# Performance work log

Measured on AMD Instinct MI355X. Metric: run time of the kernel, lower is better.

Reference implementation:

```python
import jax, jax.numpy as jnp
import numpy as np

B, Q, T, D, FD, H, N, FF = 64, 64, 448, 512, 1024, 8, 2, 2048
S = Q + T
DH = D // H
EPS = 1e-12


def _ln(x, g, b):
    m = jnp.mean(x, -1, keepdims=True)
    v = jnp.mean((x - m) ** 2, -1, keepdims=True)
    return (x - m) / jnp.sqrt(v + EPS) * g + b


def _sinusoidal(n_pos, dim):
    j = np.arange(dim)
    pos = np.arange(n_pos)[:, None]
    angle = pos / np.power(10000.0, 2 * (j // 2) / dim)
    pe = np.zeros((n_pos, dim), dtype=np.float32)
    pe[:, 0::2] = np.sin(angle[:, 0::2])
    pe[:, 1::2] = np.cos(angle[:, 1::2])
    return jnp.asarray(pe)


def setup_inputs() -> dict:
    key = jax.random.key(0)
    ks = iter(jax.random.split(key, 40))
    s = 0.02
    rn = lambda *shape: jax.random.normal(next(ks), shape, jnp.float32) * s
    inp = {
        'video': jax.random.normal(next(ks), (B, T, FD), jnp.float32),
        'question': jax.random.normal(next(ks), (B, Q, D), jnp.float32),
        'mask': jnp.ones((B, S), jnp.int32),
        'pos_emb': _sinusoidal(S, D),
        'mod_emb': rn(2, D),
        'Wv': rn(FD, D), 'bv': jnp.zeros((D,), jnp.float32),
        'nv_g': jnp.ones((D,), jnp.float32), 'nv_b': jnp.zeros((D,), jnp.float32),
        'emb_g': jnp.ones((D,), jnp.float32), 'emb_b': jnp.zeros((D,), jnp.float32),
        'Wq': rn(N, D, D), 'bq': jnp.zeros((N, D), jnp.float32),
        'Wk': rn(N, D, D), 'bk': jnp.zeros((N, D), jnp.float32),
        'Wva': rn(N, D, D), 'bva': jnp.zeros((N, D), jnp.float32),
        'Wo': rn(N, D, D), 'bo': jnp.zeros((N, D), jnp.float32),
        'ln1_g': jnp.ones((N, D), jnp.float32), 'ln1_b': jnp.zeros((N, D), jnp.float32),
        'W1': rn(N, D, FF), 'b1': jnp.zeros((N, FF), jnp.float32),
        'W2': rn(N, FF, D), 'b2': jnp.zeros((N, D), jnp.float32),
        'ln2_g': jnp.ones((N, D), jnp.float32), 'ln2_b': jnp.zeros((N, D), jnp.float32),
    }
    return inp


def reference(video, question, mask, pos_emb, mod_emb, Wv, bv, nv_g, nv_b,
              emb_g, emb_b, Wq, bq, Wk, bk, Wva, bva, Wo, bo,
              ln1_g, ln1_b, W1, b1, W2, b2, ln2_g, ln2_b):
    # project + norm video features
    v = _ln(video @ Wv + bv, nv_g, nv_b)                      # [B,T,D]
    x = jnp.concatenate([question, v], axis=1)                # [B,S,D]
    mod_ids = jnp.concatenate([jnp.zeros(Q, jnp.int32), jnp.ones(T, jnp.int32)])
    x = x + pos_emb[None] + mod_emb[mod_ids][None]
    x = _ln(x, emb_g, emb_b)

    pad = (mask == 0)[:, None, None, :]                       # [B,1,1,S]
    scale = 1.0 / jnp.sqrt(jnp.asarray(DH, x.dtype))
    split = lambda t: t.reshape(B, S, H, DH).transpose(0, 2, 1, 3)  # [B,H,S,DH]

    for i in range(N):
        q = split(x @ Wq[i] + bq[i]) * scale
        k = split(x @ Wk[i] + bk[i])
        vv = split(x @ Wva[i] + bva[i])
        scores = jnp.einsum('bhqd,bhkd->bhqk', q, k)          # [B,H,S,S]
        scores = jnp.where(pad, -jnp.inf, scores)
        w = jax.nn.softmax(scores, axis=-1)
        ctx = jnp.einsum('bhqk,bhkd->bhqd', w, vv)
        ctx = ctx.transpose(0, 2, 1, 3).reshape(B, S, D)
        x = _ln(ctx @ Wo[i] + bo[i] + x, ln1_g[i], ln1_b[i])
        h = jax.nn.gelu(x @ W1[i] + b1[i], approximate=False)
        x = _ln(h @ W2[i] + b2[i] + x, ln2_g[i], ln2_b[i])
    return x
```

## Files before the change

kernel.cpp:

```cpp
#include <hip/hip_runtime.h>
#include <hip/hip_bf16.h>
#include <stdint.h>

#define Bb 64
#define Qq 64
#define Tt 448
#define Dd 512
#define FDd 1024
#define Hh 8
#define NL 2
#define FFf 2048
#define Ss 512
#define DHh 64

typedef unsigned short u16;
typedef __bf16 bf16x8 __attribute__((ext_vector_type(8)));
typedef float f32x4 __attribute__((ext_vector_type(4)));
typedef u16 u16x4 __attribute__((ext_vector_type(4)));

__device__ __forceinline__ float bf2f(u16 u) { return __uint_as_float(((uint32_t)u) << 16); }
__device__ __forceinline__ u16 f2bfu(float f) {
    __bf16 h = (__bf16)f;
    return __builtin_bit_cast(unsigned short, h);
}
__device__ __forceinline__ float ldx(const void* p, long i, int isbf) {
    return isbf ? bf2f(((const u16*)p)[i]) : ((const float*)p)[i];
}
__device__ __forceinline__ float geluf(float v) {
    float u = v * (1.0f + 0.044715f * v * v) * -1.5957691216057308f;
    return v / (1.0f + __expf(u));
}
__device__ __forceinline__ void gload16(const void* g, void* l) {
    __builtin_amdgcn_global_load_lds((const __attribute__((address_space(1))) void*)g,
                                     (__attribute__((address_space(3))) void*)l, 16, 0, 0);
}
#define MFMA16(a, b, c) __builtin_amdgcn_mfma_f32_16x16x32_bf16(a, b, c, 0, 0, 0)

__global__ void probe_kernel(const void* pos_emb, int* flag) {
    if (threadIdx.x == 0) {
        uint32_t w = *(const uint32_t*)pos_emb;
        *flag = (w == 0x3F800000u) ? 1 : 0;
    }
}

__global__ void convert_kernel(const void* __restrict__ src, u16* __restrict__ dst, long n,
                               const int* __restrict__ flag) {
    const int isbf = *flag;
    if (isbf) return;
    long i = (long)blockIdx.x * blockDim.x + threadIdx.x;
    long stride = (long)gridDim.x * blockDim.x;
    for (; i < n; i += stride) {
        dst[i] = f2bfu(((const float*)src)[i]);
    }
}

__global__ void transpose_kernel(const void* __restrict__ src, u16* __restrict__ dst,
                                 int R, int C, long elem_off, const int* __restrict__ flag) {
    __shared__ u16 tile[32][33];
    const int isbf = *flag;
    const int c0 = blockIdx.x * 32, r0 = blockIdx.y * 32;
    const int tx = threadIdx.x, ty = threadIdx.y;
#pragma unroll
    for (int i = 0; i < 32; i += 8) {
        long idx = elem_off + (long)(r0 + ty + i) * C + (c0 + tx);
        tile[ty + i][tx] = isbf ? ((const u16*)src)[idx] : f2bfu(((const float*)src)[idx]);
    }
    __syncthreads();
#pragma unroll
    for (int i = 0; i < 32; i += 8) {
        dst[(long)(c0 + ty + i) * R + (r0 + tx)] = tile[tx][ty + i];
    }
}

__global__ void transpose4_kernel(const void* __restrict__ s0, const void* __restrict__ s1,
                                  const void* __restrict__ s2, const void* __restrict__ s3,
                                  u16* __restrict__ d0p, u16* __restrict__ d1p,
                                  u16* __restrict__ d2p, u16* __restrict__ d3p, long elem_off,
                                  const int* __restrict__ flag) {
    __shared__ u16 tile[32][33];
    const int isbf = *flag;
    const int z = blockIdx.z;
    const void* src = (z == 0) ? s0 : (z == 1) ? s1 : (z == 2) ? s2 : s3;
    u16* dst = (z == 0) ? d0p : (z == 1) ? d1p : (z == 2) ? d2p : d3p;
    const int c0 = blockIdx.x * 32, r0 = blockIdx.y * 32;
    const int tx = threadIdx.x, ty = threadIdx.y;
#pragma unroll
    for (int i = 0; i < 32; i += 8) {
        long idx = elem_off + (long)(r0 + ty + i) * Dd + (c0 + tx);
        tile[ty + i][tx] = isbf ? ((const u16*)src)[idx] : f2bfu(((const float*)src)[idx]);
    }
    __syncthreads();
#pragma unroll
    for (int i = 0; i < 32; i += 8) {
        dst[(long)(c0 + ty + i) * Dd + (r0 + tx)] = tile[tx][ty + i];
    }
}

template <int MH>
__device__ __forceinline__ void ld_a(bf16x8 (&af)[4][2], const u16* sa, int wm, int col16,
                                     int cp0, int cp1) {
#pragma unroll
    for (int mi = 0; mi < 4; mi++) {
        int rr = wm * 128 + MH * 64 + mi * 16 + col16;
        af[mi][0] = *(const bf16x8*)&sa[rr * 64 + cp0 * 8];
        af[mi][1] = *(const bf16x8*)&sa[rr * 64 + cp1 * 8];
    }
}
template <int NH>
__device__ __forceinline__ void ld_b(bf16x8 (&bfr)[2][2][2], const u16* sb, int wn, int col16,
                                     int cp0, int cp1) {
#pragma unroll
    for (int ni = 0; ni < 2; ni++) {
        int rr = wn * 64 + NH * 32 + ni * 16 + col16;
        bfr[NH][ni][0] = *(const bf16x8*)&sb[rr * 64 + cp0 * 8];
        bfr[NH][ni][1] = *(const bf16x8*)&sb[rr * 64 + cp1 * 8];
    }
}
template <int MH, int NH>
__device__ __forceinline__ void mma4(f32x4 (&acc)[8][4], const bf16x8 (&af)[4][2],
                                     const bf16x8 (&bfr)[2][2][2]) {
#pragma unroll
    for (int mi = 0; mi < 4; mi++)
#pragma unroll
        for (int ni = 0; ni < 2; ni++)
#pragma unroll
            for (int ks = 0; ks < 2; ks++)
                acc[MH * 4 + mi][NH * 2 + ni] =
                    MFMA16(af[mi][ks], bfr[NH][ni][ks], acc[MH * 4 + mi][NH * 2 + ni]);
}

#define PH_TAIL(MH, NH)                                       \
    __builtin_amdgcn_sched_barrier(0);                        \
    __builtin_amdgcn_s_barrier();                             \
    asm volatile("s_waitcnt lgkmcnt(0)" ::: "memory");        \
    __builtin_amdgcn_sched_barrier(0);                        \
    __builtin_amdgcn_s_setprio(1);                            \
    mma4<MH, NH>(acc, af, bfr);                               \
    __builtin_amdgcn_s_setprio(0);                            \
    __builtin_amdgcn_sched_barrier(0);

template <int MODE, int KK>
__global__ __launch_bounds__(512) void gemm256(const u16* __restrict__ A,
                                               const void* __restrict__ Araw,
                                               const u16* __restrict__ Bt,
                                               const void* __restrict__ bias, long bias_off,
                                               void* __restrict__ out, int M, int N,
                                               const int* __restrict__ flag) {
    constexpr int NT = KK / 64;
    __shared__ __align__(16) u16 sA2[2][16384];
    __shared__ __align__(16) u16 sB2[2][16384];
    const int tid = threadIdx.x;
    const int lane = tid & 63, wave = tid >> 6;
    const int wm = wave >> 2, wn = wave & 3;
    const int col16 = lane & 15, quad = lane >> 4;
    const int cp0 = quad ^ (col16 & 7);
    const int cp1 = cp0 ^ 4;
    const long m0 = (long)blockIdx.y * 256;
    const long n0 = (long)blockIdx.x * 256;
    const int isbf = *flag;
    const u16* Ap = (Araw && isbf) ? (const u16*)Araw : A;

    const int g = (tid & 7) ^ ((tid >> 3) & 7);
    const u16* agbase = Ap + (m0 + (tid >> 3)) * KK + g * 8;
    const u16* bgbase = Bt + (n0 + (tid >> 3)) * KK + g * 8;

    auto stA = [&](int kt2, int q) {
        if (kt2 < NT)
            gload16(agbase + (long)q * (64LL * KK) + (long)kt2 * 64,
                    &sA2[kt2 & 1][q * 4096 + wave * 512]);
    };
    auto stB = [&](int kt2, int q) {
        if (kt2 < NT)
            gload16(bgbase + (long)q * (64LL * KK) + (long)kt2 * 64,
                    &sB2[kt2 & 1][q * 4096 + wave * 512]);
    };

    f32x4 acc[8][4];
#pragma unroll
    for (int i = 0; i < 8; i++)
#pragma unroll
        for (int j = 0; j < 4; j++) acc[i][j] = (f32x4){0.f, 0.f, 0.f, 0.f};

    stA(0, 0); stA(0, 1); stA(0, 2); stA(0, 3);
    stB(0, 0); stB(0, 1); stB(0, 2); stB(0, 3);
    stB(1, 0); stB(1, 1); stB(1, 2); stB(1, 3);
    asm volatile("s_waitcnt vmcnt(4)" ::: "memory");
    __builtin_amdgcn_s_barrier();

    bf16x8 af[4][2];
    bf16x8 bfr[2][2][2];

#pragma unroll 2
    for (int kt = 0; kt < NT; ++kt) {
        const u16* sa = &sA2[kt & 1][0];
        const u16* sb = &sB2[kt & 1][0];
        ld_a<0>(af, sa, wm, col16, cp0, cp1);
        ld_b<0>(bfr, sb, wn, col16, cp0, cp1);
        stA(kt + 1, 0);
        stA(kt + 1, 1);
        PH_TAIL(0, 0)
        __builtin_amdgcn_s_barrier();
        ld_b<1>(bfr, sb, wn, col16, cp0, cp1);
        stA(kt + 1, 2);
        stA(kt + 1, 3);
        PH_TAIL(0, 1)
        __builtin_amdgcn_s_barrier();
        ld_a<1>(af, sa, wm, col16, cp0, cp1);
        stB(kt + 2, 0);
        stB(kt + 2, 1);
        PH_TAIL(1, 0)
        __builtin_amdgcn_s_barrier();
        stB(kt + 2, 2);
        stB(kt + 2, 3);
        PH_TAIL(1, 1)
        if (kt + 2 < NT)
            asm volatile("s_waitcnt vmcnt(4)" ::: "memory");
        else if (kt + 1 < NT)
            asm volatile("s_waitcnt vmcnt(0)" ::: "memory");
        __builtin_amdgcn_s_barrier();
    }

    float bb[4];
#pragma unroll
    for (int ni = 0; ni < 4; ni++)
        bb[ni] = ldx(bias, bias_off + n0 + wn * 64 + ni * 16 + col16, isbf);
#pragma unroll
    for (int mi = 0; mi < 8; mi++) {
#pragma unroll
        for (int ni = 0; ni < 4; ni++) {
            long col = n0 + wn * 64 + ni * 16 + col16;
#pragma unroll
            for (int r = 0; r < 4; r++) {
                long row = m0 + wm * 128 + mi * 16 + quad * 4 + r;
                float v = acc[mi][ni][r] + bb[ni];
                if (MODE == 0) {
                    ((u16*)out)[row * N + col] = f2bfu(v);
                } else {
                    ((u16*)out)[row * N + col] = f2bfu(geluf(v));
                }
            }
        }
    }
}

__global__ __launch_bounds__(256) void qkv_kernel(const u16* __restrict__ A,
                                                  const u16* __restrict__ Bt,
                                                  const void* __restrict__ bq,
                                                  const void* __restrict__ bk,
                                                  const void* __restrict__ bva, long boff,
                                                  u16* __restrict__ qb, u16* __restrict__ kb,
                                                  u16* __restrict__ vtb,
                                                  const int* __restrict__ flag) {
    __shared__ __align__(16) u16 sA[128 * 32];
    __shared__ __align__(16) u16 sB[128 * 32];
    const int tid = threadIdx.x;
    const int lane = tid & 63, wave = tid >> 6;
    const int wm = wave >> 1, wn = wave & 1;
    const int col16 = lane & 15, quad = lane >> 4;
    const long m0 = (long)blockIdx.y * 128;
    const long n0 = (long)blockIdx.x * 128;
    const int KK = Dd;

    f32x4 acc[4][4];
#pragma unroll
    for (int i = 0; i < 4; i++)
#pragma unroll
        for (int j = 0; j < 4; j++) acc[i][j] = (f32x4){0.f, 0.f, 0.f, 0.f};

    const int sr = tid >> 2, skq = tid & 3;
    const int ssg = skq ^ ((sr >> 1) & 3);
    const int sr2 = (tid + 256) >> 2;
    const int ssg2 = skq ^ ((sr2 >> 1) & 3);

#pragma unroll
    for (int k0 = 0; k0 < KK; k0 += 32) {
        __syncthreads();
        {
            int lbase = (wave * 64) * 8;
            gload16(&A[(m0 + sr) * KK + k0 + ssg * 8], &sA[lbase]);
            gload16(&Bt[(n0 + sr) * KK + k0 + ssg * 8], &sB[lbase]);
            int lbase2 = (256 + wave * 64) * 8;
            gload16(&A[(m0 + sr2) * KK + k0 + ssg2 * 8], &sA[lbase2]);
            gload16(&Bt[(n0 + sr2) * KK + k0 + ssg2 * 8], &sB[lbase2]);
        }
        __syncthreads();
        bf16x8 af[4], bfv[4];
#pragma unroll
        for (int mi = 0; mi < 4; mi++) {
            int rr = wm * 64 + mi * 16 + col16;
            af[mi] = *(const bf16x8*)&sA[(rr * 4 + (quad ^ ((rr >> 1) & 3))) * 8];
        }
#pragma unroll
        for (int ni = 0; ni < 4; ni++) {
            int rr = wn * 64 + ni * 16 + col16;
            bfv[ni] = *(const bf16x8*)&sB[(rr * 4 + (quad ^ ((rr >> 1) & 3))) * 8];
        }
#pragma unroll
        for (int mi = 0; mi < 4; mi++)
#pragma unroll
            for (int ni = 0; ni < 4; ni++)
                acc[mi][ni] = MFMA16(af[mi], bfv[ni], acc[mi][ni]);
    }

    const int isbf = *flag;
    const int region = (int)(n0 >> 9);
    const void* bias = (region == 0) ? bq : (region == 1) ? bk : bva;
    float bb[4];
#pragma unroll
    for (int ni = 0; ni < 4; ni++) {
        long col = n0 + wn * 64 + ni * 16 + col16;
        bb[ni] = ldx(bias, boff + (col & 511), isbf);
    }

#pragma unroll
    for (int mi = 0; mi < 4; mi++) {
#pragma unroll
        for (int ni = 0; ni < 4; ni++) {
            long col = n0 + wn * 64 + ni * 16 + col16;
            long cc = col & 511;
            long h = cc >> 6, dh = cc & 63;
            long row0 = m0 + wm * 64 + mi * 16 + quad * 4;
            long b = row0 >> 9, s0 = row0 & 511;
            if (region == 0) {
#pragma unroll
                for (int r = 0; r < 4; r++)
                    qb[(((b * 8 + h) * 512) + s0 + r) * 64 + dh] =
                        f2bfu((acc[mi][ni][r] + bb[ni]) * 0.125f);
            } else if (region == 1) {
#pragma unroll
                for (int r = 0; r < 4; r++)
                    kb[(((b * 8 + h) * 512) + s0 + r) * 64 + dh] = f2bfu(acc[mi][ni][r] + bb[ni]);
            } else {
                u16x4 pk;
#pragma unroll
                for (int r = 0; r < 4; r++) pk[r] = f2bfu(acc[mi][ni][r] + bb[ni]);
                *(u16x4*)&vtb[(((b * 8 + h) * 64) + dh) * 512 + s0] = pk;
            }
        }
    }
}

__device__ __forceinline__ float wredsum(float v) {
#pragma unroll
    for (int off = 1; off < 64; off <<= 1) v += __shfl_xor(v, off);
    return v;
}
__device__ __forceinline__ void ln8(float v[8]) {
    float s = 0.f;
#pragma unroll
    for (int j = 0; j < 8; j++) s += v[j];
    s = wredsum(s);
    float m = s * (1.0f / 512.0f);
    float q = 0.f;
#pragma unroll
    for (int j = 0; j < 8; j++) {
        v[j] -= m;
        q += v[j] * v[j];
    }
    q = wredsum(q);
    float inv = rsqrtf(q * (1.0f / 512.0f) + 1e-12f);
#pragma unroll
    for (int j = 0; j < 8; j++) v[j] *= inv;
}

__global__ __launch_bounds__(256) void embed_kernel(
    const void* __restrict__ question, const void* __restrict__ pos, const void* __restrict__ mod,
    const u16* __restrict__ tmp, const void* __restrict__ nvg, const void* __restrict__ nvb,
    const void* __restrict__ eg, const void* __restrict__ eb, u16* __restrict__ x,
    const int* __restrict__ flag) {
    const int isbf = *flag;
    const int wave = threadIdx.x >> 6, lane = threadIdx.x & 63;
    const long row = (long)blockIdx.x * 4 + wave;
    const int b = (int)(row >> 9), s = (int)(row & 511);
    const int d0 = lane * 4, d1 = 256 + lane * 4;
    float v[8];
    if (s < Qq) {
        long base = ((long)b * Qq + s) * Dd;
#pragma unroll
        for (int j = 0; j < 4; j++) {
            v[j] = ldx(question, base + d0 + j, isbf);
            v[4 + j] = ldx(question, base + d1 + j, isbf);
        }
    } else {
        const u16* tr = tmp + ((long)b * Tt + (s - Qq)) * Dd;
        u16x4 f0 = *(const u16x4*)(tr + d0);
        u16x4 f1 = *(const u16x4*)(tr + d1);
#pragma unroll
        for (int j = 0; j < 4; j++) {
            v[j] = bf2f(f0[j]);
            v[4 + j] = bf2f(f1[j]);
        }
        ln8(v);
#pragma unroll
        for (int j = 0; j < 4; j++) {
            v[j] = v[j] * ldx(nvg, d0 + j, isbf) + ldx(nvb, d0 + j, isbf);
            v[4 + j] = v[4 + j] * ldx(nvg, d1 + j, isbf) + ldx(nvb, d1 + j, isbf);
        }
    }
    const int mid = (s < Qq) ? 0 : 1;
#pragma unroll
    for (int j = 0; j < 4; j++) {
        v[j] += ldx(pos, (long)s * Dd + d0 + j, isbf) + ldx(mod, (long)mid * Dd + d0 + j, isbf);
        v[4 + j] += ldx(pos, (long)s * Dd + d1 + j, isbf) + ldx(mod, (long)mid * Dd + d1 + j, isbf);
    }
    ln8(v);
#pragma unroll
    for (int j = 0; j < 4; j++) {
        x[row * Dd + d0 + j] = f2bfu(v[j] * ldx(eg, d0 + j, isbf) + ldx(eb, d0 + j, isbf));
        x[row * Dd + d1 + j] = f2bfu(v[4 + j] * ldx(eg, d1 + j, isbf) + ldx(eb, d1 + j, isbf));
    }
}

__global__ __launch_bounds__(256) void add_ln_kernel(const u16* __restrict__ tmp,
                                                     const u16* __restrict__ xin,
                                                     const void* __restrict__ g,
                                                     const void* __restrict__ bta, long goff,
                                                     void* __restrict__ dst, int dst_is_final,
                                                     const int* __restrict__ flag) {
    const int isbf = *flag;
    const int wave = threadIdx.x >> 6, lane = threadIdx.x & 63;
    const long row = (long)blockIdx.x * 4 + wave;
// ... 151 lines not shown
        for (int dt = 0; dt < 4; dt++) {
#pragma unroll
            for (int r = 0; r < 4; r++) {
                float v = acc[t][dt][r] / accl[t][r];
                int sq = qbase + t * 16 + quad * 4 + r;
                int d = h * 64 + dt * 16 + col16;
                ctx[((long)b * Ss + sq) * Dd + d] = f2bfu(v);
            }
        }
}

extern "C" void kernel_launch(void* const* d_in, const int* in_sizes, int n_in, void* d_out,
                              int out_size, void* d_ws, size_t ws_size, hipStream_t stream) {
    const void* video = d_in[0];
    const void* question = d_in[1];
    const int* mask = (const int*)d_in[2];
    const void* pos_emb = d_in[3];
    const void* mod_emb = d_in[4];
    const void* Wv = d_in[5];
    const void* bv = d_in[6];
    const void* nv_g = d_in[7];
    const void* nv_b = d_in[8];
    const void* emb_g = d_in[9];
    const void* emb_b = d_in[10];
    const void* Wq = d_in[11];
    const void* bq = d_in[12];
    const void* Wk = d_in[13];
    const void* bk = d_in[14];
    const void* Wva = d_in[15];
    const void* bva = d_in[16];
    const void* Wo = d_in[17];
    const void* bo = d_in[18];
    const void* ln1_g = d_in[19];
    const void* ln1_b = d_in[20];
    const void* W1 = d_in[21];
    const void* b1 = d_in[22];
    const void* W2 = d_in[23];
    const void* b2 = d_in[24];
    const void* ln2_g = d_in[25];
    const void* ln2_b = d_in[26];

    char* wsb = (char*)d_ws;
    size_t off = 0;
    auto alloc = [&](size_t bytes) -> void* {
        void* p = (void*)(wsb + off);
        off += (bytes + 4095) & ~((size_t)4095);
        return p;
    };
    int* flag = (int*)alloc(16);
    u16* WvT = (u16*)alloc((size_t)Dd * FDd * 2);
    u16 *WqkvT[NL], *WoT[NL], *W1T[NL], *W2T[NL];
    for (int i = 0; i < NL; i++) {
        WqkvT[i] = (u16*)alloc((size_t)3 * Dd * Dd * 2);
        WoT[i] = (u16*)alloc((size_t)Dd * Dd * 2);
        W1T[i] = (u16*)alloc((size_t)FFf * Dd * 2);
        W2T[i] = (u16*)alloc((size_t)Dd * FFf * 2);
    }
    u16* x = (u16*)alloc((size_t)Bb * Ss * Dd * 2);
    u16* tmp = (u16*)alloc((size_t)Bb * Ss * Dd * 2);
    char* uni = (char*)alloc((size_t)134217728);
    u16* videob = (u16*)uni;
    u16* qb = (u16*)uni;
    u16* kb = (u16*)(uni + 33554432);
    u16* vtb = (u16*)(uni + 67108864);
    u16* ctxb = (u16*)(uni + 100663296);
    u16* hb = (u16*)uni;

    dim3 tb(32, 8);

    probe_kernel<<<dim3(1), dim3(64), 0, stream>>>(pos_emb, flag);
    convert_kernel<<<dim3(8192), dim3(256), 0, stream>>>(video, videob, (long)Bb * Tt * FDd, flag);

    transpose_kernel<<<dim3(Dd / 32, FDd / 32), tb, 0, stream>>>(Wv, WvT, FDd, Dd, 0L, flag);
    for (int i = 0; i < NL; i++) {
        transpose4_kernel<<<dim3(Dd / 32, Dd / 32, 4), tb, 0, stream>>>(
            Wq, Wk, Wva, Wo, WqkvT[i], WqkvT[i] + (size_t)Dd * Dd,
            WqkvT[i] + (size_t)2 * Dd * Dd, WoT[i], (long)i * Dd * Dd, flag);
        transpose_kernel<<<dim3(FFf / 32, Dd / 32), tb, 0, stream>>>(W1, W1T[i], Dd, FFf,
                                                                     (long)i * Dd * FFf, flag);
        transpose_kernel<<<dim3(Dd / 32, FFf / 32), tb, 0, stream>>>(W2, W2T[i], FFf, Dd,
                                                                     (long)i * FFf * Dd, flag);
    }

    gemm256<0, FDd><<<dim3(2, 112), dim3(512), 0, stream>>>(videob, video, WvT, bv, 0L, tmp,
                                                            Bb * Tt, Dd, flag);
    embed_kernel<<<dim3((Bb * Ss) / 4), dim3(256), 0, stream>>>(question, pos_emb, mod_emb, tmp,
                                                                nv_g, nv_b, emb_g, emb_b, x, flag);

    for (int i = 0; i < NL; i++) {
        qkv_kernel<<<dim3(12, 256), dim3(256), 0, stream>>>(x, WqkvT[i], bq, bk, bva,
                                                            (long)i * Dd, qb, kb, vtb, flag);
        flash_kernel<<<dim3(2048), dim3(256), 0, stream>>>(qb, kb, vtb, mask, ctxb);
        gemm256<0, Dd><<<dim3(2, 128), dim3(512), 0, stream>>>(ctxb, nullptr, WoT[i], bo,
                                                               (long)i * Dd, tmp, Bb * Ss, Dd,
                                                               flag);
        add_ln_kernel<<<dim3((Bb * Ss) / 4), dim3(256), 0, stream>>>(tmp, x, ln1_g, ln1_b,
                                                                     (long)i * Dd, x, 0, flag);
        gemm256<1, Dd><<<dim3(8, 128), dim3(512), 0, stream>>>(x, nullptr, W1T[i], b1,
                                                               (long)i * FFf, hb, Bb * Ss, FFf,
                                                               flag);
        gemm256<0, FFf><<<dim3(2, 128), dim3(512), 0, stream>>>(hb, nullptr, W2T[i], b2,
                                                                (long)i * Dd, tmp, Bb * Ss, Dd,
                                                                flag);
        void* dst = (i == NL - 1) ? d_out : (void*)x;
        add_ln_kernel<<<dim3((Bb * Ss) / 4), dim3(256), 0, stream>>>(
            tmp, x, ln2_g, ln2_b, (long)i * Dd, dst, (i == NL - 1) ? 1 : 0, flag);
    }
    (void)in_sizes; (void)n_in; (void)out_size; (void)ws_size;
}
```

Before: 1.339 ms.

## Use 256x256 pipelined GEMM for QKV and add XCD-aware block swizzle

Replaces the simple 128x128 single-buffered QKV GEMM with the same double-buffered 256x256 pipelined core used by the other GEMMs, shared through a macro. All GEMMs now launch a 1D grid and remap block IDs so that consecutive M tiles land on the same XCD, aiming to improve L2 reuse of A rows and weight tiles. The output width becomes a template parameter. Risks include fewer blocks for QKV (768 vs 3072) reducing occupancy, and the remap assumes M/256 is divisible by 8.

```diff
diff --git a/kernel.cpp b/kernel.cpp
--- a/kernel.cpp
+++ b/kernel.cpp
@@ -129,96 +129,100 @@
                     MFMA16(af[mi][ks], bfr[NH][ni][ks], acc[MH * 4 + mi][NH * 2 + ni]);
 }
 
-#define PH_TAIL(MH, NH)                                       \
-    __builtin_amdgcn_sched_barrier(0);                        \
-    __builtin_amdgcn_s_barrier();                             \
-    asm volatile("s_waitcnt lgkmcnt(0)" ::: "memory");        \
-    __builtin_amdgcn_sched_barrier(0);                        \
-    __builtin_amdgcn_s_setprio(1);                            \
-    mma4<MH, NH>(acc, af, bfr);                               \
-    __builtin_amdgcn_s_setprio(0);                            \
+#define PH_TAIL(MH, NH)                                \
+    __builtin_amdgcn_sched_barrier(0);                 \
+    __builtin_amdgcn_s_barrier();                      \
+    asm volatile("s_waitcnt lgkmcnt(0)" ::: "memory"); \
+    __builtin_amdgcn_sched_barrier(0);                 \
+    __builtin_amdgcn_s_setprio(1);                     \
+    mma4<MH, NH>(acc, af, bfr);                        \
+    __builtin_amdgcn_s_setprio(0);                     \
     __builtin_amdgcn_sched_barrier(0);
 
-template <int MODE, int KK>
+#define GEMM256_CORE(APTR, BPTR, KK_, NT_)                                                    \
+    const int tid = threadIdx.x;                                                              \
+    const int lane = tid & 63, wave = tid >> 6;                                               \
+    const int wm = wave >> 2, wn = wave & 3;                                                  \
+    const int col16 = lane & 15, quad = lane >> 4;                                            \
+    const int cp0 = quad ^ (col16 & 7);                                                       \
+    const int cp1 = cp0 ^ 4;                                                                  \
+    const int g = (tid & 7) ^ ((tid >> 3) & 7);                                               \
+    const u16* agbase = (APTR) + (m0 + (tid >> 3)) * (KK_) + g * 8;                           \
+    const u16* bgbase = (BPTR) + (n0 + (tid >> 3)) * (KK_) + g * 8;                           \
+    auto stA = [&](int kt2, int q) {                                                          \
+        if (kt2 < (NT_))                                                                      \
+            gload16(agbase + (long)q * (64LL * (KK_)) + (long)kt2 * 64,                       \
+                    &sA2[kt2 & 1][q * 4096 + wave * 512]);                                    \
+    };                                                                                        \
+    auto stB = [&](int kt2, int q) {                                                          \
+        if (kt2 < (NT_))                                                                      \
+            gload16(bgbase + (long)q * (64LL * (KK_)) + (long)kt2 * 64,                       \
+                    &sB2[kt2 & 1][q * 4096 + wave * 512]);                                    \
+    };                                                                                        \
+    f32x4 acc[8][4];                                                                          \
+    _Pragma("unroll") for (int i = 0; i < 8; i++) _Pragma("unroll") for (int j = 0; j < 4;    \
+                                                                         j++) acc[i][j] =    \
+        (f32x4){0.f, 0.f, 0.f, 0.f};                                                          \
+    stA(0, 0); stA(0, 1); stA(0, 2); stA(0, 3);                                               \
+    stB(0, 0); stB(0, 1); stB(0, 2); stB(0, 3);                                               \
+    stB(1, 0); stB(1, 1); stB(1, 2); stB(1, 3);                                               \
+    asm volatile("s_waitcnt vmcnt(4)" ::: "memory");                                          \
+    __builtin_amdgcn_s_barrier();                                                             \
+    bf16x8 af[4][2];                                                                          \
+    bf16x8 bfr[2][2][2];                                                                      \
+    _Pragma("unroll 2") for (int kt = 0; kt < (NT_); ++kt) {                                  \
+        const u16* sa = &sA2[kt & 1][0];                                                      \
+        const u16* sb = &sB2[kt & 1][0];                                                      \
+        ld_a<0>(af, sa, wm, col16, cp0, cp1);                                                 \
+        ld_b<0>(bfr, sb, wn, col16, cp0, cp1);                                                \
+        stA(kt + 1, 0);                                                                       \
+        stA(kt + 1, 1);                                                                       \
+        PH_TAIL(0, 0)                                                                         \
+        __builtin_amdgcn_s_barrier();                                                         \
+        ld_b<1>(bfr, sb, wn, col16, cp0, cp1);                                                \
+        stA(kt + 1, 2);                                                                       \
+        stA(kt + 1, 3);                                                                       \
+        PH_TAIL(0, 1)                                                                         \
+        __builtin_amdgcn_s_barrier();                                                         \
+        ld_a<1>(af, sa, wm, col16, cp0, cp1);                                                 \
+        stB(kt + 2, 0);                                                                       \
+        stB(kt + 2, 1);                                                                       \
+        PH_TAIL(1, 0)                                                                         \
+        __builtin_amdgcn_s_barrier();                                                         \
+        stB(kt + 2, 2);                                                                       \
+        stB(kt + 2, 3);                                                                       \
+        PH_TAIL(1, 1)                                                                         \
+        if (kt + 2 < (NT_))                                                                   \
+            asm volatile("s_waitcnt vmcnt(4)" ::: "memory");                                  \
+        else if (kt + 1 < (NT_))                                                              \
+            asm volatile("s_waitcnt vmcnt(0)" ::: "memory");                                  \
+        __builtin_amdgcn_s_barrier();                                                         \
+    }
+
+template <int MODE, int KK, int NN>
 __global__ __launch_bounds__(512) void gemm256(const u16* __restrict__ A,
                                                const void* __restrict__ Araw,
                                                const u16* __restrict__ Bt,
                                                const void* __restrict__ bias, long bias_off,
-                                               void* __restrict__ out, int M, int N,
+                                               void* __restrict__ out, int M,
                                                const int* __restrict__ flag) {
     constexpr int NT = KK / 64;
+    constexpr int nbn = NN >> 8;
     __shared__ __align__(16) u16 sA2[2][16384];
     __shared__ __align__(16) u16 sB2[2][16384];
-    const int tid = threadIdx.x;
-    const int lane = tid & 63, wave = tid >> 6;
-    const int wm = wave >> 2, wn = wave & 3;
-    const int col16 = lane & 15, quad = lane >> 4;
-    const int cp0 = quad ^ (col16 & 7);
-    const int cp1 = cp0 ^ 4;
-    const long m0 = (long)blockIdx.y * 256;
-    const long n0 = (long)blockIdx.x * 256;
     const int isbf = *flag;
     const u16* Ap = (Araw && isbf) ? (const u16*)Araw : A;
 
-    const int g = (tid & 7) ^ ((tid >> 3) & 7);
-    const u16* agbase = Ap + (m0 + (tid >> 3)) * KK + g * 8;
-    const u16* bgbase = Bt + (n0 + (tid >> 3)) * KK + g * 8;
-
-    auto stA = [&](int kt2, int q) {
-        if (kt2 < NT)
-            gload16(agbase + (long)q * (64LL * KK) + (long)kt2 * 64,
-                    &sA2[kt2 & 1][q * 4096 + wave * 512]);
-    };
-    auto stB = [&](int kt2, int q) {
-        if (kt2 < NT)
-            gload16(bgbase + (long)q * (64LL * KK) + (long)kt2 * 64,
-                    &sB2[kt2 & 1][q * 4096 + wave * 512]);
-    };
-
-    f32x4 acc[8][4];
-#pragma unroll
-    for (int i = 0; i < 8; i++)
-#pragma unroll
-        for (int j = 0; j < 4; j++) acc[i][j] = (f32x4){0.f, 0.f, 0.f, 0.f};
-
-    stA(0, 0); stA(0, 1); stA(0, 2); stA(0, 3);
-    stB(0, 0); stB(0, 1); stB(0, 2); stB(0, 3);
-    stB(1, 0); stB(1, 1); stB(1, 2); stB(1, 3);
-    asm volatile("s_waitcnt vmcnt(4)" ::: "memory");
-    __builtin_amdgcn_s_barrier();
-
-    bf16x8 af[4][2];
-    bf16x8 bfr[2][2][2];
-
-#pragma unroll 2
-    for (int kt = 0; kt < NT; ++kt) {
-        const u16* sa = &sA2[kt & 1][0];
-        const u16* sb = &sB2[kt & 1][0];
-        ld_a<0>(af, sa, wm, col16, cp0, cp1);
-        ld_b<0>(bfr, sb, wn, col16, cp0, cp1);
-        stA(kt + 1, 0);
-        stA(kt + 1, 1);
-        PH_TAIL(0, 0)
-        __builtin_amdgcn_s_barrier();
-        ld_b<1>(bfr, sb, wn, col16, cp0, cp1);
-        stA(kt + 1, 2);
-        stA(kt + 1, 3);
-        PH_TAIL(0, 1)
-        __builtin_amdgcn_s_barrier();
-        ld_a<1>(af, sa, wm, col16, cp0, cp1);
-        stB(kt + 2, 0);
-        stB(kt + 2, 1);
-        PH_TAIL(1, 0)
-        __builtin_amdgcn_s_barrier();
-        stB(kt + 2, 2);
-        stB(kt + 2, 3);
-        PH_TAIL(1, 1)
-        if (kt + 2 < NT)
-            asm volatile("s_waitcnt vmcnt(4)" ::: "memory");
-        else if (kt + 1 < NT)
-            asm volatile("s_waitcnt vmcnt(0)" ::: "memory");
-        __builtin_amdgcn_s_barrier();
-    }
+    const int bid = blockIdx.x;
+    const int xcd = bid & 7;
+    const int loc = bid >> 3;
+    const int chunk = (M >> 8) >> 3;
+    const int mloc = loc / nbn;
+    const int nloc = loc - mloc * nbn;
+    const long m0 = (long)(xcd * chunk + mloc) << 8;
+    const long n0 = (long)nloc << 8;
+
+    GEMM256_CORE(Ap, Bt, KK, NT)
 
     float bb[4];
 #pragma unroll
@@ -234,75 +238,41 @@
                 long row = m0 + wm * 128 + mi * 16 + quad * 4 + r;
                 float v = acc[mi][ni][r] + bb[ni];
                 if (MODE == 0) {
-                    ((u16*)out)[row * N + col] = f2bfu(v);
+                    ((u16*)out)[row * NN + col] = f2bfu(v);
                 } else {
-                    ((u16*)out)[row * N + col] = f2bfu(geluf(v));
+                    ((u16*)out)[row * NN + col] = f2bfu(geluf(v));
                 }
             }
         }
     }
 }
 
-__global__ __launch_bounds__(256) void qkv_kernel(const u16* __restrict__ A,
-                                                  const u16* __restrict__ Bt,
-                                                  const void* __restrict__ bq,
-                                                  const void* __restrict__ bk,
-                                                  const void* __restrict__ bva, long boff,
-                                                  u16* __restrict__ qb, u16* __restrict__ kb,
-                                                  u16* __restrict__ vtb,
-                                                  const int* __restrict__ flag) {
-    __shared__ __align__(16) u16 sA[128 * 32];
-    __shared__ __align__(16) u16 sB[128 * 32];
-    const int tid = threadIdx.x;
-    const int lane = tid & 63, wave = tid >> 6;
-    const int wm = wave >> 1, wn = wave & 1;
-    const int col16 = lane & 15, quad = lane >> 4;
-    const long m0 = (long)blockIdx.y * 128;
-    const long n0 = (long)blockIdx.x * 128;
-    const int KK = Dd;
-
-    f32x4 acc[4][4];
-#pragma unroll
-    for (int i = 0; i < 4; i++)
-#pragma unroll
-        for (int j = 0; j < 4; j++) acc[i][j] = (f32x4){0.f, 0.f, 0.f, 0.f};
-
-    const int sr = tid >> 2, skq = tid & 3;
-    const int ssg = skq ^ ((sr >> 1) & 3);
-    const int sr2 = (tid + 256) >> 2;
-    const int ssg2 = skq ^ ((sr2 >> 1) & 3);
-
-#pragma unroll
-    for (int k0 = 0; k0 < KK; k0 += 32) {
-        __syncthreads();
-        {
-            int lbase = (wave * 64) * 8;
-            gload16(&A[(m0 + sr) * KK + k0 + ssg * 8], &sA[lbase]);
-            gload16(&Bt[(n0 + sr) * KK + k0 + ssg * 8], &sB[lbase]);
-            int lbase2 = (256 + wave * 64) * 8;
-            gload16(&A[(m0 + sr2) * KK + k0 + ssg2 * 8], &sA[lbase2]);
-            gload16(&Bt[(n0 + sr2) * KK + k0 + ssg2 * 8], &sB[lbase2]);
-        }
-        __syncthreads();
-        bf16x8 af[4], bfv[4];
-#pragma unroll
-        for (int mi = 0; mi < 4; mi++) {
-            int rr = wm * 64 + mi * 16 + col16;
-            af[mi] = *(const bf16x8*)&sA[(rr * 4 + (quad ^ ((rr >> 1) & 3))) * 8];
-        }
-#pragma unroll
-        for (int ni = 0; ni < 4; ni++) {
-            int rr = wn * 64 + ni * 16 + col16;
-            bfv[ni] = *(const bf16x8*)&sB[(rr * 4 + (quad ^ ((rr >> 1) & 3))) * 8];
-        }
-#pragma unroll
-        for (int mi = 0; mi < 4; mi++)
-#pragma unroll
-            for (int ni = 0; ni < 4; ni++)
-                acc[mi][ni] = MFMA16(af[mi], bfv[ni], acc[mi][ni]);
-    }
-
+__global__ __launch_bounds__(512) void qkv256(const u16* __restrict__ A,
+                                              const u16* __restrict__ Bt,
+                                              const void* __restrict__ bq,
+                                              const void* __restrict__ bk,
+                                              const void* __restrict__ bva, long boff,
+                                              u16* __restrict__ qb, u16* __restrict__ kb,
+                                              u16* __restrict__ vtb,
+                                              const int* __restrict__ flag) {
+    constexpr int KK = Dd;
+    constexpr int NT = KK / 64;
+    constexpr int nbn = 6;
+    __shared__ __align__(16) u16 sA2[2][16384];
+    __shared__ __align__(16) u16 sB2[2][16384];
     const int isbf = *flag;
+
+    const int bid = blockIdx.x;
+    const int xcd = bid & 7;
+    const int loc = bid >> 3;
+    const int chunk = 16;
+    const int mloc = loc / nbn;
+    const int nloc = loc - mloc * nbn;
+    const long m0 = (long)(xcd * chunk + mloc) << 8;
+    const long n0 = (long)nloc << 8;
+
+    GEMM256_CORE(A, Bt, KK, NT)
+
     const int region = (int)(n0 >> 9);
     const void* bias = (region == 0) ? bq : (region == 1) ? bk : bva;
     float bb[4];
@@ -313,13 +283,13 @@
     }
 
 #pragma unroll
-    for (int mi = 0; mi < 4; mi++) {
+    for (int mi = 0; mi < 8; mi++) {
 #pragma unroll
         for (int ni = 0; ni < 4; ni++) {
             long col = n0 + wn * 64 + ni * 16 + col16;
             long cc = col & 511;
             long h = cc >> 6, dh = cc & 63;
-            long row0 = m0 + wm * 64 + mi * 16 + quad * 4;
+            long row0 = m0 + wm * 128 + mi * 16 + quad * 4;
             long b = row0 >> 9, s0 = row0 & 511;
             if (region == 0) {
 #pragma unroll
@@ -654,26 +624,26 @@
                                                                      (long)i * FFf * Dd, flag);
     }
 
-    gemm256<0, FDd><<<dim3(2, 112), dim3(512), 0, stream>>>(videob, video, WvT, bv, 0L, tmp,
-                                                            Bb * Tt, Dd, flag);
+    gemm256<0, FDd, Dd><<<dim3(112 * 2), dim3(512), 0, stream>>>(videob, video, WvT, bv, 0L, tmp,
+                                                                 Bb * Tt, flag);
     embed_kernel<<<dim3((Bb * Ss) / 4), dim3(256), 0, stream>>>(question, pos_emb, mod_emb, tmp,
                                                                 nv_g, nv_b, emb_g, emb_b, x, flag);
 
     for (int i = 0; i < NL; i++) {
-        qkv_kernel<<<dim3(12, 256), dim3(256), 0, stream>>>(x, WqkvT[i], bq, bk, bva,
-                                                            (long)i * Dd, qb, kb, vtb, flag);
+        qkv256<<<dim3(128 * 6), dim3(512), 0, stream>>>(x, WqkvT[i], bq, bk, bva, (long)i * Dd,
+                                                        qb, kb, vtb, flag);
         flash_kernel<<<dim3(2048), dim3(256), 0, stream>>>(qb, kb, vtb, mask, ctxb);
-        gemm256<0, Dd><<<dim3(2, 128), dim3(512), 0, stream>>>(ctxb, nullptr, WoT[i], bo,
-                                                               (long)i * Dd, tmp, Bb * Ss, Dd,
-                                                               flag);
+        gemm256<0, Dd, Dd><<<dim3(128 * 2), dim3(512), 0, stream>>>(ctxb, nullptr, WoT[i], bo,
+                                                                    (long)i * Dd, tmp, Bb * Ss,
+                                                                    flag);
         add_ln_kernel<<<dim3((Bb * Ss) / 4), dim3(256), 0, stream>>>(tmp, x, ln1_g, ln1_b,
                                                                      (long)i * Dd, x, 0, flag);
-        gemm256<1, Dd><<<dim3(8, 128), dim3(512), 0, stream>>>(x, nullptr, W1T[i], b1,
-                                                               (long)i * FFf, hb, Bb * Ss, FFf,
-                                                               flag);
-        gemm256<0, FFf><<<dim3(2, 128), dim3(512), 0, stream>>>(hb, nullptr, W2T[i], b2,
-                                                                (long)i * Dd, tmp, Bb * Ss, Dd,
-                                                                flag);
+        gemm256<1, Dd, FFf><<<dim3(128 * 8), dim3(512), 0, stream>>>(x, nullptr, W1T[i], b1,
+                                                                     (long)i * FFf, hb, Bb * Ss,
+                                                                     flag);
+        gemm256<0, FFf, Dd><<<dim3(128 * 2), dim3(512), 0, stream>>>(hb, nullptr, W2T[i], b2,
+                                                                     (long)i * Dd, tmp, Bb * Ss,
+                                                                     flag);
         void* dst = (i == NL - 1) ? d_out : (void*)x;
         add_ln_kernel<<<dim3((Bb * Ss) / 4), dim3(256), 0, stream>>>(
             tmp, x, ln2_g, ln2_b, (long)i * Dd, dst, (i == NL - 1) ? 1 : 0, flag);
```

Result: faster. 1.281 ms (-4.3%).

## Unify GEMMs into persistent XCD-aware 256x256 kernel with QKV epilogue and prefetch

Applied to the files above, without the earlier changes.

Replaces the separate 128x128 QKV kernel with the 256x256 pipelined GEMM, using a new epilogue mode that scatters Q (pre-scaled), K and transposed V. Block indices are remapped so each XCD works on a contiguous band of M. The W1 GEMM makes each block loop over four M tiles, reusing the pipeline and emitting an epilogue per tile. LDS fragment reads are issued earlier, with partial lgkmcnt waits and a second A-fragment buffer, to overlap them with MFMA. The aims are better L2 locality, higher MFMA efficiency for QKV and less LDS latency exposure, at the cost of more registers and fewer blocks for W1.

```diff
diff --git a/kernel.cpp b/kernel.cpp
--- a/kernel.cpp
+++ b/kernel.cpp
@@ -97,13 +97,13 @@
 }
 
 template <int MH>
-__device__ __forceinline__ void ld_a(bf16x8 (&af)[4][2], const u16* sa, int wm, int col16,
+__device__ __forceinline__ void ld_a(bf16x8 (&dst)[4][2], const u16* sa, int wm, int col16,
                                      int cp0, int cp1) {
 #pragma unroll
     for (int mi = 0; mi < 4; mi++) {
         int rr = wm * 128 + MH * 64 + mi * 16 + col16;
-        af[mi][0] = *(const bf16x8*)&sa[rr * 64 + cp0 * 8];
-        af[mi][1] = *(const bf16x8*)&sa[rr * 64 + cp1 * 8];
+        dst[mi][0] = *(const bf16x8*)&sa[rr * 64 + cp0 * 8];
+        dst[mi][1] = *(const bf16x8*)&sa[rr * 64 + cp1 * 8];
     }
 }
 template <int NH>
@@ -117,7 +117,7 @@
     }
 }
 template <int MH, int NH>
-__device__ __forceinline__ void mma4(f32x4 (&acc)[8][4], const bf16x8 (&af)[4][2],
+__device__ __forceinline__ void mma4(f32x4 (&acc)[8][4], const bf16x8 (&a)[4][2],
                                      const bf16x8 (&bfr)[2][2][2]) {
 #pragma unroll
     for (int mi = 0; mi < 4; mi++)
@@ -126,27 +126,28 @@
 #pragma unroll
             for (int ks = 0; ks < 2; ks++)
                 acc[MH * 4 + mi][NH * 2 + ni] =
-                    MFMA16(af[mi][ks], bfr[NH][ni][ks], acc[MH * 4 + mi][NH * 2 + ni]);
-}
-
-#define PH_TAIL(MH, NH)                                       \
+                    MFMA16(a[mi][ks], bfr[NH][ni][ks], acc[MH * 4 + mi][NH * 2 + ni]);
+}
+
+#define PH_CNT(MH, NH, AARR, CNT)                             \
     __builtin_amdgcn_sched_barrier(0);                        \
     __builtin_amdgcn_s_barrier();                             \
-    asm volatile("s_waitcnt lgkmcnt(0)" ::: "memory");        \
+    asm volatile("s_waitcnt lgkmcnt(" #CNT ")" ::: "memory"); \
     __builtin_amdgcn_sched_barrier(0);                        \
     __builtin_amdgcn_s_setprio(1);                            \
-    mma4<MH, NH>(acc, af, bfr);                               \
+    mma4<MH, NH>(acc, AARR, bfr);                             \
     __builtin_amdgcn_s_setprio(0);                            \
     __builtin_amdgcn_sched_barrier(0);
 
-template <int MODE, int KK>
-__global__ __launch_bounds__(512) void gemm256(const u16* __restrict__ A,
-                                               const void* __restrict__ Araw,
-                                               const u16* __restrict__ Bt,
-                                               const void* __restrict__ bias, long bias_off,
-                                               void* __restrict__ out, int M, int N,
-                                               const int* __restrict__ flag) {
+template <int MODE, int KK, int NN, int MSUB>
+__global__ __launch_bounds__(512) void gemm256(
+    const u16* __restrict__ A, const void* __restrict__ Araw, const u16* __restrict__ Bt,
+    const void* __restrict__ b0, const void* __restrict__ b1, const void* __restrict__ b2,
+    long boff, void* __restrict__ o0, void* __restrict__ o1, void* __restrict__ o2, int M,
+    const int* __restrict__ flag) {
     constexpr int NT = KK / 64;
+    constexpr int TOT = NT * MSUB;
+    constexpr int nbn = NN >> 8;
     __shared__ __align__(16) u16 sA2[2][16384];
     __shared__ __align__(16) u16 sB2[2][16384];
     const int tid = threadIdx.x;
@@ -155,24 +156,36 @@
     const int col16 = lane & 15, quad = lane >> 4;
     const int cp0 = quad ^ (col16 & 7);
     const int cp1 = cp0 ^ 4;
-    const long m0 = (long)blockIdx.y * 256;
-    const long n0 = (long)blockIdx.x * 256;
     const int isbf = *flag;
     const u16* Ap = (Araw && isbf) ? (const u16*)Araw : A;
+
+    const int bid = blockIdx.x;
+    const int xcd = bid & 7;
+    const int loc = bid >> 3;
+    const int nbm = M / (256 * MSUB);
+    const int chunk = nbm >> 3;
+    const int mloc = loc / nbn;
+    const int nloc = loc - mloc * nbn;
+    const long m0 = (long)(xcd * chunk + mloc) * (256L * MSUB);
+    const long n0 = (long)nloc << 8;
 
     const int g = (tid & 7) ^ ((tid >> 3) & 7);
     const u16* agbase = Ap + (m0 + (tid >> 3)) * KK + g * 8;
     const u16* bgbase = Bt + (n0 + (tid >> 3)) * KK + g * 8;
 
-    auto stA = [&](int kt2, int q) {
-        if (kt2 < NT)
-            gload16(agbase + (long)q * (64LL * KK) + (long)kt2 * 64,
-                    &sA2[kt2 & 1][q * 4096 + wave * 512]);
+    auto stA = [&](int s2, int q) {
+        if (s2 < TOT) {
+            const long mt = s2 / NT;
+            const long k0 = (long)(s2 & (NT - 1)) * 64;
+            gload16(agbase + mt * (256LL * KK) + (long)q * (64LL * KK) + k0,
+                    &sA2[s2 & 1][q * 4096 + wave * 512]);
+        }
     };
-    auto stB = [&](int kt2, int q) {
-        if (kt2 < NT)
-            gload16(bgbase + (long)q * (64LL * KK) + (long)kt2 * 64,
-                    &sB2[kt2 & 1][q * 4096 + wave * 512]);
+    auto stB = [&](int s2, int q) {
+        if (s2 < TOT) {
+            const long k0 = (long)(s2 & (NT - 1)) * 64;
+            gload16(bgbase + (long)q * (64LL * KK) + k0, &sB2[s2 & 1][q * 4096 + wave * 512]);
+        }
     };
 
     f32x4 acc[8][4];
@@ -180,6 +193,62 @@
     for (int i = 0; i < 8; i++)
 #pragma unroll
         for (int j = 0; j < 4; j++) acc[i][j] = (f32x4){0.f, 0.f, 0.f, 0.f};
+
+    const void* bias;
+    int region = 0;
+    if constexpr (MODE == 2) {
+        region = (int)(n0 >> 9);
+        bias = (region == 0) ? b0 : (region == 1) ? b1 : b2;
+    } else {
+        bias = b0;
+    }
+    float bb[4];
+#pragma unroll
+    for (int ni = 0; ni < 4; ni++) {
+        long col = n0 + wn * 64 + ni * 16 + col16;
+        bb[ni] = ldx(bias, boff + (MODE == 2 ? (col & 511) : col), isbf);
+    }
+
+    auto epi = [&](int mt) {
+        const long m0e = m0 + (long)mt * 256;
+#pragma unroll
+        for (int mi = 0; mi < 8; mi++) {
+#pragma unroll
+            for (int ni = 0; ni < 4; ni++) {
+                long col = n0 + wn * 64 + ni * 16 + col16;
+                if constexpr (MODE == 2) {
+                    long cc = col & 511;
+                    long h = cc >> 6, dh = cc & 63;
+                    long row0 = m0e + wm * 128 + mi * 16 + quad * 4;
+                    long b = row0 >> 9, s0 = row0 & 511;
+                    if (region == 0) {
+#pragma unroll
+                        for (int r = 0; r < 4; r++)
+                            ((u16*)o0)[(((b * 8 + h) * 512) + s0 + r) * 64 + dh] =
+                                f2bfu((acc[mi][ni][r] + bb[ni]) * 0.125f);
+                    } else if (region == 1) {
+#pragma unroll
+                        for (int r = 0; r < 4; r++)
+                            ((u16*)o1)[(((b * 8 + h) * 512) + s0 + r) * 64 + dh] =
+                                f2bfu(acc[mi][ni][r] + bb[ni]);
+                    } else {
+                        u16x4 pk;
+#pragma unroll
+                        for (int r = 0; r < 4; r++) pk[r] = f2bfu(acc[mi][ni][r] + bb[ni]);
+                        *(u16x4*)&((u16*)o2)[(((b * 8 + h) * 64) + dh) * 512 + s0] = pk;
+                    }
+                } else {
+#pragma unroll
+                    for (int r = 0; r < 4; r++) {
+                        long row = m0e + wm * 128 + mi * 16 + quad * 4 + r;
+                        float v = acc[mi][ni][r] + bb[ni];
+                        ((u16*)o0)[row * NN + col] = f2bfu(MODE == 1 ? geluf(v) : v);
+                    }
+                }
+                acc[mi][ni] = (f32x4){0.f, 0.f, 0.f, 0.f};
+            }
+        }
+    };
 
     stA(0, 0); stA(0, 1); stA(0, 2); stA(0, 3);
     stB(0, 0); stB(0, 1); stB(0, 2); stB(0, 3);
@@ -188,155 +257,41 @@
     __builtin_amdgcn_s_barrier();
 
     bf16x8 af[4][2];
+    bf16x8 ag[4][2];
     bf16x8 bfr[2][2][2];
 
 #pragma unroll 2
-    for (int kt = 0; kt < NT; ++kt) {
-        const u16* sa = &sA2[kt & 1][0];
-        const u16* sb = &sB2[kt & 1][0];
+    for (int s = 0; s < TOT; ++s) {
+        const u16* sa = &sA2[s & 1][0];
+        const u16* sb = &sB2[s & 1][0];
         ld_a<0>(af, sa, wm, col16, cp0, cp1);
         ld_b<0>(bfr, sb, wn, col16, cp0, cp1);
-        stA(kt + 1, 0);
-        stA(kt + 1, 1);
-        PH_TAIL(0, 0)
+        __builtin_amdgcn_sched_barrier(0);
+        ld_b<1>(bfr, sb, wn, col16, cp0, cp1);
+        __builtin_amdgcn_sched_barrier(0);
+        stA(s + 1, 0);
+        stA(s + 1, 1);
+        PH_CNT(0, 0, af, 4)
         __builtin_amdgcn_s_barrier();
-        ld_b<1>(bfr, sb, wn, col16, cp0, cp1);
-        stA(kt + 1, 2);
-        stA(kt + 1, 3);
-        PH_TAIL(0, 1)
+        ld_a<1>(ag, sa, wm, col16, cp0, cp1);
+        __builtin_amdgcn_sched_barrier(0);
+        stA(s + 1, 2);
+        stA(s + 1, 3);
+        PH_CNT(0, 1, af, 8)
         __builtin_amdgcn_s_barrier();
-        ld_a<1>(af, sa, wm, col16, cp0, cp1);
-        stB(kt + 2, 0);
-        stB(kt + 2, 1);
-        PH_TAIL(1, 0)
+        stB(s + 2, 0);
+        stB(s + 2, 1);
+        PH_CNT(1, 0, ag, 0)
         __builtin_amdgcn_s_barrier();
-        stB(kt + 2, 2);
-        stB(kt + 2, 3);
-        PH_TAIL(1, 1)
-        if (kt + 2 < NT)
+        stB(s + 2, 2);
+        stB(s + 2, 3);
+        PH_CNT(1, 1, ag, 0)
+        if (s + 2 < TOT)
             asm volatile("s_waitcnt vmcnt(4)" ::: "memory");
-        else if (kt + 1 < NT)
+        else if (s + 1 < TOT)
             asm volatile("s_waitcnt vmcnt(0)" ::: "memory");
         __builtin_amdgcn_s_barrier();
-    }
-
-    float bb[4];
-#pragma unroll
-    for (int ni = 0; ni < 4; ni++)
-        bb[ni] = ldx(bias, bias_off + n0 + wn * 64 + ni * 16 + col16, isbf);
-#pragma unroll
-    for (int mi = 0; mi < 8; mi++) {
-#pragma unroll
-        for (int ni = 0; ni < 4; ni++) {
-            long col = n0 + wn * 64 + ni * 16 + col16;
-#pragma unroll
-            for (int r = 0; r < 4; r++) {
-                long row = m0 + wm * 128 + mi * 16 + quad * 4 + r;
-                float v = acc[mi][ni][r] + bb[ni];
-                if (MODE == 0) {
-                    ((u16*)out)[row * N + col] = f2bfu(v);
-                } else {
-                    ((u16*)out)[row * N + col] = f2bfu(geluf(v));
-                }
-            }
-        }
-    }
-}
-
-__global__ __launch_bounds__(256) void qkv_kernel(const u16* __restrict__ A,
-                                                  const u16* __restrict__ Bt,
-                                                  const void* __restrict__ bq,
-                                                  const void* __restrict__ bk,
-                                                  const void* __restrict__ bva, long boff,
-                                                  u16* __restrict__ qb, u16* __restrict__ kb,
-                                                  u16* __restrict__ vtb,
-                                                  const int* __restrict__ flag) {
-    __shared__ __align__(16) u16 sA[128 * 32];
-    __shared__ __align__(16) u16 sB[128 * 32];
-    const int tid = threadIdx.x;
-    const int lane = tid & 63, wave = tid >> 6;
-    const int wm = wave >> 1, wn = wave & 1;
-    const int col16 = lane & 15, quad = lane >> 4;
-    const long m0 = (long)blockIdx.y * 128;
-    const long n0 = (long)blockIdx.x * 128;
-    const int KK = Dd;
-
-    f32x4 acc[4][4];
-#pragma unroll
-    for (int i = 0; i < 4; i++)
-#pragma unroll
-        for (int j = 0; j < 4; j++) acc[i][j] = (f32x4){0.f, 0.f, 0.f, 0.f};
-
-    const int sr = tid >> 2, skq = tid & 3;
-    const int ssg = skq ^ ((sr >> 1) & 3);
-    const int sr2 = (tid + 256) >> 2;
-    const int ssg2 = skq ^ ((sr2 >> 1) & 3);
-
-#pragma unroll
-    for (int k0 = 0; k0 < KK; k0 += 32) {
-        __syncthreads();
-        {
-            int lbase = (wave * 64) * 8;
-            gload16(&A[(m0 + sr) * KK + k0 + ssg * 8], &sA[lbase]);
-            gload16(&Bt[(n0 + sr) * KK + k0 + ssg * 8], &sB[lbase]);
-            int lbase2 = (256 + wave * 64) * 8;
-            gload16(&A[(m0 + sr2) * KK + k0 + ssg2 * 8], &sA[lbase2]);
-            gload16(&Bt[(n0 + sr2) * KK + k0 + ssg2 * 8], &sB[lbase2]);
-        }
-        __syncthreads();
-        bf16x8 af[4], bfv[4];
-#pragma unroll
-        for (int mi = 0; mi < 4; mi++) {
-            int rr = wm * 64 + mi * 16 + col16;
-            af[mi] = *(const bf16x8*)&sA[(rr * 4 + (quad ^ ((rr >> 1) & 3))) * 8];
-        }
-#pragma unroll
-        for (int ni = 0; ni < 4; ni++) {
-            int rr = wn * 64 + ni * 16 + col16;
-            bfv[ni] = *(const bf16x8*)&sB[(rr * 4 + (quad ^ ((rr >> 1) & 3))) * 8];
-        }
-#pragma unroll
-        for (int mi = 0; mi < 4; mi++)
-#pragma unroll
-            for (int ni = 0; ni < 4; ni++)
-                acc[mi][ni] = MFMA16(af[mi], bfv[ni], acc[mi][ni]);
-    }
-
-    const int isbf = *flag;
-    const int region = (int)(n0 >> 9);
-    const void* bias = (region == 0) ? bq : (region == 1) ? bk : bva;
-    float bb[4];
-#pragma unroll
-    for (int ni = 0; ni < 4; ni++) {
-        long col = n0 + wn * 64 + ni * 16 + col16;
-        bb[ni] = ldx(bias, boff + (col & 511), isbf);
-    }
-
-#pragma unroll
-    for (int mi = 0; mi < 4; mi++) {
-#pragma unroll
-        for (int ni = 0; ni < 4; ni++) {
-            long col = n0 + wn * 64 + ni * 16 + col16;
-            long cc = col & 511;
-            long h = cc >> 6, dh = cc & 63;
-            long row0 = m0 + wm * 64 + mi * 16 + quad * 4;
-            long b = row0 >> 9, s0 = row0 & 511;
-            if (region == 0) {
-#pragma unroll
-                for (int r = 0; r < 4; r++)
-                    qb[(((b * 8 + h) * 512) + s0 + r) * 64 + dh] =
-                        f2bfu((acc[mi][ni][r] + bb[ni]) * 0.125f);
-            } else if (region == 1) {
-#pragma unroll
-                for (int r = 0; r < 4; r++)
-                    kb[(((b * 8 + h) * 512) + s0 + r) * 64 + dh] = f2bfu(acc[mi][ni][r] + bb[ni]);
-            } else {
-                u16x4 pk;
-#pragma unroll
-                for (int r = 0; r < 4; r++) pk[r] = f2bfu(acc[mi][ni][r] + bb[ni]);
-                *(u16x4*)&vtb[(((b * 8 + h) * 64) + dh) * 512 + s0] = pk;
-            }
-        }
+        if ((s & (NT - 1)) == NT - 1) epi(s / NT);
     }
 }
 
@@ -654,26 +609,26 @@
                                                                      (long)i * FFf * Dd, flag);
     }
 
-    gemm256<0, FDd><<<dim3(2, 112), dim3(512), 0, stream>>>(videob, video, WvT, bv, 0L, tmp,
-                                                            Bb * Tt, Dd, flag);
+    gemm256<0, FDd, Dd, 1><<<dim3(224), dim3(512), 0, stream>>>(
+        videob, video, WvT, bv, nullptr, nullptr, 0L, tmp, nullptr, nullptr, Bb * Tt, flag);
     embed_kernel<<<dim3((Bb * Ss) / 4), dim3(256), 0, stream>>>(question, pos_emb, mod_emb, tmp,
                                                                 nv_g, nv_b, emb_g, emb_b, x, flag);
 
     for (int i = 0; i < NL; i++) {
-        qkv_kernel<<<dim3(12, 256), dim3(256), 0, stream>>>(x, WqkvT[i], bq, bk, bva,
-                                                            (long)i * Dd, qb, kb, vtb, flag);
+        gemm256<2, Dd, 1536, 1><<<dim3(768), dim3(512), 0, stream>>>(
+            x, nullptr, WqkvT[i], bq, bk, bva, (long)i * Dd, qb, kb, vtb, Bb * Ss, flag);
         flash_kernel<<<dim3(2048), dim3(256), 0, stream>>>(qb, kb, vtb, mask, ctxb);
-        gemm256<0, Dd><<<dim3(2, 128), dim3(512), 0, stream>>>(ctxb, nullptr, WoT[i], bo,
-                                                               (long)i * Dd, tmp, Bb * Ss, Dd,
-                                                               flag);
+        gemm256<0, Dd, Dd, 1><<<dim3(256), dim3(512), 0, stream>>>(
+            ctxb, nullptr, WoT[i], bo, nullptr, nullptr, (long)i * Dd, tmp, nullptr, nullptr,
+            Bb * Ss, flag);
         add_ln_kernel<<<dim3((Bb * Ss) / 4), dim3(256), 0, stream>>>(tmp, x, ln1_g, ln1_b,
                                                                      (long)i * Dd, x, 0, flag);
-        gemm256<1, Dd><<<dim3(8, 128), dim3(512), 0, stream>>>(x, nullptr, W1T[i], b1,
-                                                               (long)i * FFf, hb, Bb * Ss, FFf,
-                                                               flag);
-        gemm256<0, FFf><<<dim3(2, 128), dim3(512), 0, stream>>>(hb, nullptr, W2T[i], b2,
-                                                                (long)i * Dd, tmp, Bb * Ss, Dd,
-                                                                flag);
+        gemm256<1, Dd, FFf, 4><<<dim3(256), dim3(512), 0, stream>>>(
+            x, nullptr, W1T[i], b1, nullptr, nullptr, (long)i * FFf, hb, nullptr, nullptr,
+            Bb * Ss, flag);
+        gemm256<0, FFf, Dd, 1><<<dim3(256), dim3(512), 0, stream>>>(
+            hb, nullptr, W2T[i], b2, nullptr, nullptr, (long)i * Dd, tmp, nullptr, nullptr,
+            Bb * Ss, flag);
         void* dst = (i == NL - 1) ? d_out : (void*)x;
         add_ln_kernel<<<dim3((Bb * Ss) / 4), dim3(256), 0, stream>>>(
             tmp, x, ln2_g, ln2_b, (long)i * Dd, dst, (i == NL - 1) ? 1 : 0, flag);
```

After: 1.611 ms. 20.3% more time.
